# Performance work log

Measured on AMD Instinct MI355X. Metric: run time of the kernel, lower is better.

## Reference

```python
import jax, jax.numpy as jnp
import numpy as np

B, N, F_IN, E, S, L, ITERS = 1, 3072, 64, 4, 32, 3, 5  # batch, nodes, in-feats, edge types, units, layers, GGNN iters


def _gated_graph(h, edges, wz, wr, wh, uz, ur, uh, bz, br):
    # h: [B,N,S]; edges: [E,N,N] (edges[e,m,n] = edge m->n of type e); w*: [E,S,S]
    def step(h, _):
        # activation = edges.transpose(1,2) @ h  -> per-type aggregation of source-node states
        act = jnp.einsum('emn,bms->bens', edges, h)          # [B,E,N,S]
        z = jax.nn.sigmoid(jnp.einsum('bens,esk->bnk', act, wz) + h @ uz + bz)
        r = jax.nn.sigmoid(jnp.einsum('bens,esk->bnk', act, wr) + h @ ur + br)
        hh = jnp.tanh(jnp.einsum('bens,esk->bnk', act, wh) + (r * h) @ uh)
        return z * h + (1.0 - z) * hh, None
    h, _ = jax.lax.scan(step, h, None, length=ITERS)
    return h


def setup_inputs() -> dict:
    key = jax.random.key(0)
    ks = jax.random.split(key, 20)
    x_padded = jax.random.normal(ks[0], (B, N, F_IN), dtype=jnp.float32)
    x_lengths = jnp.full((B,), N, dtype=jnp.int32)
    # sparse 0/1 adjacency per edge type (graph structure), stored dense as in the original
    edges = (jax.random.uniform(ks[1], (E, N, N)) < 0.005).astype(jnp.float32)
    sd = 1.0 / np.sqrt(S)
    fc_w = jax.random.normal(ks[2], (F_IN, S), jnp.float32) / np.sqrt(F_IN)
    fc_b = jnp.zeros((S,), jnp.float32)
    wz = jax.random.normal(ks[3], (L, E, S, S), jnp.float32) * sd
    wr = jax.random.normal(ks[4], (L, E, S, S), jnp.float32) * sd
    wh = jax.random.normal(ks[5], (L, E, S, S), jnp.float32) * sd
    uz = jax.random.normal(ks[6], (L, S, S), jnp.float32) * sd
    ur = jax.random.normal(ks[7], (L, S, S), jnp.float32) * sd
    uh = jax.random.normal(ks[8], (L, S, S), jnp.float32) * sd
    bz = jnp.zeros((L, S), jnp.float32)
    br = jnp.zeros((L, S), jnp.float32)
    out_w = jax.random.normal(ks[9], (S, 5), jnp.float32) * sd
    out_b = jnp.zeros((5,), jnp.float32)
    return {"x_padded": x_padded, "x_lengths": x_lengths, "edges": edges,
            "fc_w": fc_w, "fc_b": fc_b, "wz": wz, "wr": wr, "wh": wh,
            "uz": uz, "ur": ur, "uh": uh, "bz": bz, "br": br,
            "out_w": out_w, "out_b": out_b}


def reference(x_padded, x_lengths, edges, fc_w, fc_b, wz, wr, wh, uz, ur, uh, bz, br, out_w, out_b):
    h = x_padded @ fc_w + fc_b                              # [B,N,S]
    for l in range(L):                                      # 3 stacked GatedGraph layers
        h = _gated_graph(h, edges, wz[l], wr[l], wh[l], uz[l], ur[l], uh[l], bz[l], br[l])
    y = h[:, 5] @ out_w + out_b                             # node index 5 -> [B,5]
    return jax.nn.log_softmax(y, axis=1)
```

## Files before the change

kernel.cpp:

```cpp
#include <hip/hip_runtime.h>

constexpr int N     = 3072;
constexpr int S     = 32;
constexpr int E     = 4;
constexpr int FIN   = 64;
constexpr int CAP   = 64;
constexpr int NNi   = N * N;
constexpr int DUMMY = N;
constexpr int BLK   = 256;
constexpr int TPB   = 768;
constexpr int NPB   = 12;

__device__ __forceinline__ float rl(float v, int lane) {
    return __int_as_float(__builtin_amdgcn_readlane(__float_as_int(v), lane));
}
__device__ __forceinline__ float fast_sigmoid(float x) {
    x = fminf(fmaxf(x, -30.f), 30.f);
    return 1.f / (1.f + __expf(-x));
}
__device__ __forceinline__ float fast_tanh(float x) {
    x = fminf(fmaxf(x, -15.f), 15.f);
    float e = __expf(2.f * x);
    return (e - 1.f) / (e + 1.f);
}

__device__ __forceinline__ float ld_dev(const float* p) {
    return __hip_atomic_load((float*)p, __ATOMIC_RELAXED, __HIP_MEMORY_SCOPE_AGENT);
}
__device__ __forceinline__ void st_dev(float* p, float v) {
    __hip_atomic_store(p, v, __ATOMIC_RELAXED, __HIP_MEMORY_SCOPE_AGENT);
}

__device__ __forceinline__ bool gbar(int* bar, int ph, int b) {
    __shared__ int ok;
    __syncthreads();
    if (threadIdx.x == 0) {
        int* grp  = bar + (b >> 4) * 16;
        int* root = bar + 256;
        int* go   = bar + 272;
        int old = __hip_atomic_fetch_add(grp, 1, __ATOMIC_RELAXED, __HIP_MEMORY_SCOPE_AGENT);
        if (old + 1 == ph * 16) {
            int old2 = __hip_atomic_fetch_add(root, 1, __ATOMIC_RELAXED, __HIP_MEMORY_SCOPE_AGENT);
            if (old2 + 1 == ph * 16)
                __hip_atomic_store(go, ph, __ATOMIC_RELAXED, __HIP_MEMORY_SCOPE_AGENT);
        }
        int spins = 0, okl = 1;
        while (__hip_atomic_load(go, __ATOMIC_RELAXED, __HIP_MEMORY_SCOPE_AGENT) < ph) {
            __builtin_amdgcn_s_sleep(2);
            if (++spins > 300000) { okl = 0; break; }
        }
        ok = okl;
    }
    __syncthreads();
    return ok != 0;
}

__global__ __launch_bounds__(256) void build_csr(const float* __restrict__ edges,
                                                 int* __restrict__ deg,
                                                 int* __restrict__ csr) {
    int t = blockIdx.x * 256 + threadIdx.x;
    int idx4 = t * 4;
    float4 v = *reinterpret_cast<const float4*>(edges + idx4);
    if (v.x == 0.f && v.y == 0.f && v.z == 0.f && v.w == 0.f) return;
    int e   = idx4 / NNi;
    int rem = idx4 - e * NNi;
    int m   = rem / N;
    int nb  = rem - m * N;
    float w[4] = {v.x, v.y, v.z, v.w};
    int base = e * N + nb;
    #pragma unroll
    for (int j = 0; j < 4; ++j) {
        if (w[j] != 0.f) {
            int slot = base + j;
            int pos = atomicAdd(&deg[slot], 1);
            if (pos < CAP) csr[slot * CAP + pos] = m;
        }
    }
}

struct Params {
    const float *x, *fcw, *fcb;
    const float *wz, *wr, *wh, *uz, *ur, *uh, *bz, *br;
    const float *ow, *ob;
    const int   *deg, *csr;
    int   *bar;
    float *h0, *h1, *out;
};

__global__ __launch_bounds__(TPB, 1) void fused_ggnn(Params p) {
    __shared__ __align__(16) float sW[3 * 4096];
    __shared__ __align__(16) float sU[3 * 1024];
    __shared__ float sB[64];

    const int tid  = threadIdx.x;
    const int b    = blockIdx.x;
    const int wid  = tid >> 6;
    const int lane = tid & 63;
    const int s    = lane & 31;
    const int g    = lane >> 5;
    const int n    = b * NPB + wid;

    if (tid < 32 * NPB) {
        int n0 = b * NPB + (tid >> 5);
        int s0 = tid & 31;
        float acc = p.fcb[s0];
        #pragma unroll 8
        for (int k = 0; k < FIN; ++k)
            acc = fmaf(p.x[n0 * FIN + k], p.fcw[k * S + s0], acc);
        st_dev(&p.h0[n0 * S + s0], acc);
    } else if (b == 0) {
        if (tid < 416)      st_dev(&p.h0[DUMMY * S + (tid - 384)], 0.f);
        else if (tid < 448) st_dev(&p.h1[DUMMY * S + (tid - 416)], 0.f);
    }

    const int slot1 = g * N + n;
    const int slot2 = (g + 2) * N + n;
    const int d1 = min(p.deg[slot1], CAP);
    const int d2 = min(p.deg[slot2], CAP);
    const int* __restrict__ l1 = p.csr + slot1 * CAP;
    const int* __restrict__ l2 = p.csr + slot2 * CAP;
    const int dm = max(d1, d2);

    const float* hp = p.h0;
    float*       hn = p.h1;
    float hlast = 0.f;
    int   phase = 1;

    gbar(p.bar, phase, b); phase++;

    for (int l = 0; l < 3; ++l) {
        __syncthreads();
        {
            float4* dw = (float4*)sW;
            const float4* gz = (const float4*)(p.wz + l * 4096);
            const float4* gr = (const float4*)(p.wr + l * 4096);
            const float4* gh = (const float4*)(p.wh + l * 4096);
            for (int i = tid; i < 1024; i += TPB) {
                dw[i] = gz[i]; dw[1024 + i] = gr[i]; dw[2048 + i] = gh[i];
            }
            float4* du = (float4*)sU;
            const float4* guz = (const float4*)(p.uz + l * 1024);
            const float4* gur = (const float4*)(p.ur + l * 1024);
            const float4* guh = (const float4*)(p.uh + l * 1024);
            if (tid < 256) {
                du[tid] = guz[tid]; du[256 + tid] = gur[tid]; du[512 + tid] = guh[tid];
            }
            if (tid < 64) sB[tid] = (tid < 32) ? p.bz[l * 32 + tid]
                                               : p.br[l * 32 + (tid - 32)];
        }
        __syncthreads();

        for (int it = 0; it < 5; ++it) {
            float acc0 = 0.f, acc1 = 0.f;
            for (int c = 0; c < dm; c += 4) {
                int4 ia = *reinterpret_cast<const int4*>(l1 + c);
                int4 ib = *reinterpret_cast<const int4*>(l2 + c);
                int r0 = (c + 0 < d1) ? ia.x : DUMMY;
                int r1 = (c + 1 < d1) ? ia.y : DUMMY;
                int r2 = (c + 2 < d1) ? ia.z : DUMMY;
                int r3 = (c + 3 < d1) ? ia.w : DUMMY;
                int q0 = (c + 0 < d2) ? ib.x : DUMMY;
                int q1 = (c + 1 < d2) ? ib.y : DUMMY;
                int q2 = (c + 2 < d2) ? ib.z : DUMMY;
                int q3 = (c + 3 < d2) ? ib.w : DUMMY;
                float v0 = ld_dev(hp + r0 * S + s), v1 = ld_dev(hp + r1 * S + s);
                float v2 = ld_dev(hp + r2 * S + s), v3 = ld_dev(hp + r3 * S + s);
                float u0 = ld_dev(hp + q0 * S + s), u1 = ld_dev(hp + q1 * S + s);
                float u2 = ld_dev(hp + q2 * S + s), u3 = ld_dev(hp + q3 * S + s);
                acc0 += (v0 + v1) + (v2 + v3);
                acc1 += (u0 + u1) + (u2 + u3);
            }
            const float hval = ld_dev(hp + n * S + s);

            const float* __restrict__ W1 = g ? (sW + 4096) : sW;
            const float* __restrict__ U1 = g ? (sU + 1024) : sU;
            const float* __restrict__ Wh = sW + 8192;
            float accA = sB[g * 32 + s];
            float accB = 0.f;
            float hA = 0.f, hB = 0.f;
            #pragma unroll
            for (int e = 0; e < E; ++e) {
                const float src = (e < 2) ? acc0 : acc1;
                const float* w1c = W1 + e * 1024 + s;
                const float* whc = Wh + e * 1024 + s;
                #pragma unroll
                for (int k = 0; k < 32; k += 2) {
                    float a0 = rl(src, (e & 1) * 32 + k);
                    float a1 = rl(src, (e & 1) * 32 + k + 1);
                    accA = fmaf(a0, w1c[(k)     * 32], accA);
                    accB = fmaf(a1, w1c[(k + 1) * 32], accB);
                    hA   = fmaf(a0, whc[(k)     * 32], hA);
                    hB   = fmaf(a1, whc[(k + 1) * 32], hB);
                }
            }
            #pragma unroll
            for (int k = 0; k < 32; k += 2) {
                accA = fmaf(rl(hval, k),     U1[(k)     * 32 + s], accA);
                accB = fmaf(rl(hval, k + 1), U1[(k + 1) * 32 + s], accB);
            }
            const float zr  = fast_sigmoid(accA + accB);
            const float r_s = __shfl(zr, 32 + s, 64);
            const float z_s = __shfl(zr, s, 64);
            const float rh  = r_s * hval;
            const float* __restrict__ Uh = sU + 2048;
            #pragma unroll
            for (int k = 0; k < 32; k += 2) {
                hA = fmaf(rl(rh, k),     Uh[(k)     * 32 + s], hA);
                hB = fmaf(rl(rh, k + 1), Uh[(k + 1) * 32 + s], hB);
            }
            const float hh   = fast_tanh(hA + hB);
            const float hnew = fmaf(z_s, hval - hh, hh);
            if (g == 0) st_dev(&hn[n * S + s], hnew);
            hlast = hnew;

            float* t = (float*)hp; hp = hn; hn = t;

            if (l != 2 || it != 4) {
                gbar(p.bar, phase, b); phase++;
            }
        }
    }

    if (b == 0 && wid == 5) {
        float y[5];
        #pragma unroll
        for (int j = 0; j < 5; ++j) y[j] = hlast * p.ow[s * 5 + j];
        #pragma unroll
        for (int off = 1; off < 32; off <<= 1) {
            #pragma unroll
            for (int j = 0; j < 5; ++j) y[j] += __shfl_xor(y[j], off, 64);
        }
        #pragma unroll
        for (int j = 0; j < 5; ++j) y[j] += p.ob[j];
        float m = -1e30f;
        #pragma unroll
        for (int j = 0; j < 5; ++j) m = fmaxf(m, y[j]);
        float ssum = 0.f;
        #pragma unroll
        for (int j = 0; j < 5; ++j) ssum += __expf(y[j] - m);
        float lse = m + __logf(ssum);
        #pragma unroll
        for (int j = 0; j < 5; ++j) if (lane == j) p.out[j] = y[j] - lse;
    }
}

__global__ __launch_bounds__(256) void init_h_fb(const float* __restrict__ x,
                                                 const float* __restrict__ fcw,
                                                 const float* __restrict__ fcb,
                                                 float* __restrict__ h0) {
    int t = blockIdx.x * 256 + threadIdx.x;
    int s = t & 31;
    int n = t >> 5;
    float acc = fcb[s];
    #pragma unroll 8
    for (int k = 0; k < FIN; ++k)
        acc = fmaf(x[n * FIN + k], fcw[k * S + s], acc);
    h0[n * S + s] = acc;
}

__global__ __launch_bounds__(512) void ggnn_iter_fb(
    const float* __restrict__ hprev, float* __restrict__ hnext,
    const int* __restrict__ deg, const int* __restrict__ csr,
    const float* __restrict__ wz, const float* __restrict__ wr, const float* __restrict__ wh,
    const float* __restrict__ uz, const float* __restrict__ ur, const float* __restrict__ uh,
    const float* __restrict__ bz, const float* __restrict__ br) {
    __shared__ __align__(16) float sWz[4096];
    __shared__ __align__(16) float sWr[4096];
    __shared__ __align__(16) float sWh[4096];
    __shared__ __align__(16) float sUz[1024], sUr[1024], sUh[1024];

    int tid = threadIdx.x;
    {
        float4*       dz = (float4*)sWz; const float4* gz = (const float4*)wz;
        float4*       dr = (float4*)sWr; const float4* gr = (const float4*)wr;
        float4*       dh = (float4*)sWh; const float4* gh = (const float4*)wh;
        for (int i = tid; i < 1024; i += 512) { dz[i] = gz[i]; dr[i] = gr[i]; dh[i] = gh[i]; }
        float4*       duz = (float4*)sUz; const float4* guz = (const float4*)uz;
        float4*       dur = (float4*)sUr; const float4* gur = (const float4*)ur;
        float4*       duh = (float4*)sUh; const float4* guh = (const float4*)uh;
        if (tid < 256) { duz[tid] = guz[tid]; dur[tid] = gur[tid]; duh[tid] = guh[tid]; }
    }
    __syncthreads();

    const int wid  = tid >> 6;
    const int lane = tid & 63;
    const int s    = lane & 31;
    const int g    = lane >> 5;
    const int n    = blockIdx.x * 8 + wid;

    const int d1 = min(deg[g * N + n], CAP);
    const int d2 = min(deg[(g + 2) * N + n], CAP);
    const int* __restrict__ l1 = csr + (g * N + n) * CAP;
    const int* __restrict__ l2 = csr + ((g + 2) * N + n) * CAP;
    float acc0 = 0.f, acc1 = 0.f;
    const int dmax = max(d1, d2);
    for (int i = 0; i < dmax; ++i) {
        if (i < d1) acc0 += hprev[l1[i] * S + s];
        if (i < d2) acc1 += hprev[l2[i] * S + s];
    }
    const float hval = hprev[n * S + s];

    const float* __restrict__ W1 = g ? sWr : sWz;
    const float* __restrict__ U1 = g ? sUr : sUz;
    float accA = g ? br[s] : bz[s];
    float accB = 0.f;
    float hA = 0.f, hB = 0.f;
    #pragma unroll
    for (int e = 0; e < E; ++e) {
        const float src = (e < 2) ? acc0 : acc1;
        const float* w1c = W1 + e * 1024 + s;
        const float* whc = sWh + e * 1024 + s;
        #pragma unroll
        for (int k = 0; k < 32; k += 2) {
            float a0 = rl(src, (e & 1) * 32 + k);
            float a1 = rl(src, (e & 1) * 32 + k + 1);
            accA = fmaf(a0, w1c[(k)     * 32], accA);
            accB = fmaf(a1, w1c[(k + 1) * 32], accB);
            hA   = fmaf(a0, whc[(k)     * 32], hA);
            hB   = fmaf(a1, whc[(k + 1) * 32], hB);
        }
    }
    #pragma unroll
    for (int k = 0; k < 32; k += 2) {
        accA = fmaf(rl(hval, k),     U1[(k)     * 32 + s], accA);
        accB = fmaf(rl(hval, k + 1), U1[(k + 1) * 32 + s], accB);
    }
    const float zr  = fast_sigmoid(accA + accB);
    const float r_s = __shfl(zr, 32 + s, 64);
    const float z_s = __shfl(zr, s, 64);
    const float rh  = r_s * hval;
    #pragma unroll
    for (int k = 0; k < 32; k += 2) {
        hA = fmaf(rl(rh, k),     sUh[(k)     * 32 + s], hA);
        hB = fmaf(rl(rh, k + 1), sUh[(k + 1) * 32 + s], hB);
    }
    const float hh = fast_tanh(hA + hB);
    const float hnew = fmaf(z_s, hval - hh, hh);
    if (g == 0) hnext[n * S + s] = hnew;
}

__global__ void epilogue_fb(const float* __restrict__ h,
                            const float* __restrict__ ow, const float* __restrict__ ob,
                            float* __restrict__ out) {
    int lane = threadIdx.x;
    float y = 0.f;
    if (lane < 5) {
        y = ob[lane];
        for (int k = 0; k < 32; ++k)
            y = fmaf(h[5 * S + k], ow[k * 5 + lane], y);
    }
    float m = -1e30f;
    #pragma unroll
    for (int j = 0; j < 5; ++j) m = fmaxf(m, __shfl(y, j, 64));
    float ssum = 0.f;
    #pragma unroll
    for (int j = 0; j < 5; ++j) ssum += __expf(__shfl(y, j, 64) - m);
    float lse = m + __logf(ssum);
    if (lane < 5) out[lane] = y - lse;
}

extern "C" void kernel_launch(void* const* d_in, const int* in_sizes, int n_in,
                              void* d_out, int out_size, void* d_ws, size_t ws_size,
                              hipStream_t stream) {
    const float* x     = (const float*)d_in[0];
    const float* edges = (const float*)d_in[2];
    const float* fcw   = (const float*)d_in[3];
    const float* fcb   = (const float*)d_in[4];
    const float* wz    = (const float*)d_in[5];
    const float* wr    = (const float*)d_in[6];
    const float* wh    = (const float*)d_in[7];
    const float* uz    = (const float*)d_in[8];
    const float* ur    = (const float*)d_in[9];
    const float* uh    = (const float*)d_in[10];
    const float* bz    = (const float*)d_in[11];
    const float* br    = (const float*)d_in[12];
    const float* ow    = (const float*)d_in[13];
    const float* ob    = (const float*)d_in[14];

    char* ws = (char*)d_ws;
    float* h0  = (float*)(ws);
    float* h1  = (float*)(ws + 393600);
    int*   deg = (int*)(ws + 787200);
    int*   bar = (int*)(ws + 836352);
    int*   csr = (int*)(ws + 838400);

    hipMemsetAsync(deg, 0, 49152 + 2048, stream);
    build_csr<<<36864, 256, 0, stream>>>(edges, deg, csr);

    Params p;
    p.x = x; p.fcw = fcw; p.fcb = fcb;
    p.wz = wz; p.wr = wr; p.wh = wh;
    p.uz = uz; p.ur = ur; p.uh = uh;
    p.bz = bz; p.br = br; p.ow = ow; p.ob = ob;
    p.deg = deg; p.csr = csr; p.bar = bar;
    p.h0 = h0; p.h1 = h1; p.out = (float*)d_out;

    void* args[] = { &p };
    hipError_t err = hipLaunchCooperativeKernel((const void*)fused_ggnn,
                                                dim3(BLK), dim3(TPB), args, 0, stream);
    if (err != hipSuccess) {
        init_h_fb<<<384, 256, 0, stream>>>(x, fcw, fcb, h0);
        float* ha = h0;
        float* hb = h1;
        for (int l = 0; l < 3; ++l) {
            for (int it = 0; it < 5; ++it) {
                ggnn_iter_fb<<<384, 512, 0, stream>>>(ha, hb, deg, csr,
                    wz + l * 4096, wr + l * 4096, wh + l * 4096,
                    uz + l * 1024, ur + l * 1024, uh + l * 1024,
                    bz + l * 32, br + l * 32);
                float* t = ha; ha = hb; hb = t;
            }
        }
        epilogue_fb<<<1, 64, 0, stream>>>(ha, ow, ob, (float*)d_out);
    }
}
```

Before: 464.1 us.

## Map two nodes per wave, one half-wave each, with LDS-staged GRU matvecs

Each block now runs 384 threads instead of 768. Each 64-lane wave handles two nodes, with one 32-lane half per node. That half gathers all four edge types itself and computes the z, r and candidate matvecs from activations staged in shared memory, replacing the readlane broadcasts and the cross-half shuffle. The node state stays in a register instead of being reloaded from global memory each iteration. The U matrices are now read from global memory (cache) rather than shared memory, which adds block-level syncs and more serial FMAs per thread in exchange for fewer threads and less cross-lane traffic.

```diff
diff --git a/kernel.cpp b/kernel.cpp
--- a/kernel.cpp
+++ b/kernel.cpp
@@ -8,7 +8,7 @@
 constexpr int NNi   = N * N;
 constexpr int DUMMY = N;
 constexpr int BLK   = 256;
-constexpr int TPB   = 768;
+constexpr int TPB   = 384;
 constexpr int NPB   = 12;
 
 __device__ __forceinline__ float rl(float v, int lane) {
@@ -31,8 +31,7 @@
     __hip_atomic_store(p, v, __ATOMIC_RELAXED, __HIP_MEMORY_SCOPE_AGENT);
 }
 
-__device__ __forceinline__ bool gbar(int* bar, int ph, int b) {
-    __shared__ int ok;
+__device__ __forceinline__ void gbar(int* bar, int ph, int b) {
     __syncthreads();
     if (threadIdx.x == 0) {
         int* grp  = bar + (b >> 4) * 16;
@@ -44,15 +43,13 @@
             if (old2 + 1 == ph * 16)
                 __hip_atomic_store(go, ph, __ATOMIC_RELAXED, __HIP_MEMORY_SCOPE_AGENT);
         }
-        int spins = 0, okl = 1;
+        int spins = 0;
         while (__hip_atomic_load(go, __ATOMIC_RELAXED, __HIP_MEMORY_SCOPE_AGENT) < ph) {
             __builtin_amdgcn_s_sleep(2);
-            if (++spins > 300000) { okl = 0; break; }
-        }
-        ok = okl;
+            if (++spins > 300000) break;
+        }
     }
     __syncthreads();
-    return ok != 0;
 }
 
 __global__ __launch_bounds__(256) void build_csr(const float* __restrict__ edges,
@@ -87,45 +84,77 @@
     float *h0, *h1, *out;
 };
 
+__device__ __forceinline__ float matvec(const float* __restrict__ Wg,
+                                        const float* __restrict__ Ug,
+                                        const float* __restrict__ actw,
+                                        const float* __restrict__ hw,
+                                        float bias, int s) {
+    float acc = bias, acc2 = 0.f;
+    #pragma unroll
+    for (int e = 0; e < E; ++e) {
+        const float* wc = Wg + e * 1024 + s;
+        const float* ar = actw + e * 32;
+        #pragma unroll
+        for (int k4 = 0; k4 < 8; ++k4) {
+            float4 a = *reinterpret_cast<const float4*>(ar + k4 * 4);
+            acc  = fmaf(a.x, wc[(k4 * 4 + 0) * 32], acc);
+            acc2 = fmaf(a.y, wc[(k4 * 4 + 1) * 32], acc2);
+            acc  = fmaf(a.z, wc[(k4 * 4 + 2) * 32], acc);
+            acc2 = fmaf(a.w, wc[(k4 * 4 + 3) * 32], acc2);
+        }
+    }
+    const float* uc = Ug + s;
+    #pragma unroll
+    for (int k4 = 0; k4 < 8; ++k4) {
+        float4 hv = *reinterpret_cast<const float4*>(hw + k4 * 4);
+        acc  = fmaf(hv.x, uc[(k4 * 4 + 0) * 32], acc);
+        acc2 = fmaf(hv.y, uc[(k4 * 4 + 1) * 32], acc2);
+        acc  = fmaf(hv.z, uc[(k4 * 4 + 2) * 32], acc);
+        acc2 = fmaf(hv.w, uc[(k4 * 4 + 3) * 32], acc2);
+    }
+    return acc + acc2;
+}
+
 __global__ __launch_bounds__(TPB, 1) void fused_ggnn(Params p) {
     __shared__ __align__(16) float sW[3 * 4096];
-    __shared__ __align__(16) float sU[3 * 1024];
-    __shared__ float sB[64];
+    __shared__ __align__(16) float sAct[6][2][E][32];
+    __shared__ __align__(16) float sH[6][2][32];
+    __shared__ __align__(16) float sRH[6][2][32];
 
     const int tid  = threadIdx.x;
     const int b    = blockIdx.x;
-    const int wid  = tid >> 6;
+    const int w    = tid >> 6;
     const int lane = tid & 63;
+    const int pp   = lane >> 5;
     const int s    = lane & 31;
-    const int g    = lane >> 5;
-    const int n    = b * NPB + wid;
-
-    if (tid < 32 * NPB) {
-        int n0 = b * NPB + (tid >> 5);
-        int s0 = tid & 31;
-        float acc = p.fcb[s0];
+    const int n    = b * NPB + w * 2 + pp;
+
+    float hval;
+    {
+        float acc = p.fcb[s];
         #pragma unroll 8
         for (int k = 0; k < FIN; ++k)
-            acc = fmaf(p.x[n0 * FIN + k], p.fcw[k * S + s0], acc);
-        st_dev(&p.h0[n0 * S + s0], acc);
-    } else if (b == 0) {
-        if (tid < 416)      st_dev(&p.h0[DUMMY * S + (tid - 384)], 0.f);
-        else if (tid < 448) st_dev(&p.h1[DUMMY * S + (tid - 416)], 0.f);
-    }
-
-    const int slot1 = g * N + n;
-    const int slot2 = (g + 2) * N + n;
-    const int d1 = min(p.deg[slot1], CAP);
-    const int d2 = min(p.deg[slot2], CAP);
-    const int* __restrict__ l1 = p.csr + slot1 * CAP;
-    const int* __restrict__ l2 = p.csr + slot2 * CAP;
-    const int dm = max(d1, d2);
+            acc = fmaf(p.x[n * FIN + k], p.fcw[k * S + s], acc);
+        hval = acc;
+        st_dev(&p.h0[n * S + s], acc);
+    }
+    if (b == 0) {
+        if (tid < 32)      st_dev(&p.h0[DUMMY * S + tid], 0.f);
+        else if (tid < 64) st_dev(&p.h1[DUMMY * S + (tid - 32)], 0.f);
+    }
+
+    int d[E]; const int* lst[E]; int dmx = 0;
+    #pragma unroll
+    for (int e = 0; e < E; ++e) {
+        int sl = e * N + n;
+        d[e]   = min(p.deg[sl], CAP);
+        lst[e] = p.csr + sl * CAP;
+        dmx    = max(dmx, d[e]);
+    }
 
     const float* hp = p.h0;
     float*       hn = p.h1;
-    float hlast = 0.f;
-    int   phase = 1;
-
+    int phase = 1;
     gbar(p.bar, phase, b); phase++;
 
     for (int l = 0; l < 3; ++l) {
@@ -138,93 +167,59 @@
             for (int i = tid; i < 1024; i += TPB) {
                 dw[i] = gz[i]; dw[1024 + i] = gr[i]; dw[2048 + i] = gh[i];
             }
-            float4* du = (float4*)sU;
-            const float4* guz = (const float4*)(p.uz + l * 1024);
-            const float4* gur = (const float4*)(p.ur + l * 1024);
-            const float4* guh = (const float4*)(p.uh + l * 1024);
-            if (tid < 256) {
-                du[tid] = guz[tid]; du[256 + tid] = gur[tid]; du[512 + tid] = guh[tid];
+        }
+        __syncthreads();
+
+        const float* Uz = p.uz + l * 1024;
+        const float* Ur = p.ur + l * 1024;
+        const float* Uh = p.uh + l * 1024;
+        const float  bzv = p.bz[l * 32 + s];
+        const float  brv = p.br[l * 32 + s];
+
+        for (int it = 0; it < 5; ++it) {
+            float a0 = 0.f, a1 = 0.f, a2 = 0.f, a3 = 0.f;
+            for (int c = 0; c < dmx; c += 2) {
+                int i00 = (c     < d[0]) ? lst[0][c]     : DUMMY;
+                int i01 = (c + 1 < d[0]) ? lst[0][c + 1] : DUMMY;
+                int i10 = (c     < d[1]) ? lst[1][c]     : DUMMY;
+                int i11 = (c + 1 < d[1]) ? lst[1][c + 1] : DUMMY;
+                int i20 = (c     < d[2]) ? lst[2][c]     : DUMMY;
+                int i21 = (c + 1 < d[2]) ? lst[2][c + 1] : DUMMY;
+                int i30 = (c     < d[3]) ? lst[3][c]     : DUMMY;
+                int i31 = (c + 1 < d[3]) ? lst[3][c + 1] : DUMMY;
+                float v00 = ld_dev(hp + i00 * S + s), v01 = ld_dev(hp + i01 * S + s);
+                float v10 = ld_dev(hp + i10 * S + s), v11 = ld_dev(hp + i11 * S + s);
+                float v20 = ld_dev(hp + i20 * S + s), v21 = ld_dev(hp + i21 * S + s);
+                float v30 = ld_dev(hp + i30 * S + s), v31 = ld_dev(hp + i31 * S + s);
+                a0 += v00 + v01; a1 += v10 + v11;
+                a2 += v20 + v21; a3 += v30 + v31;
             }
-            if (tid < 64) sB[tid] = (tid < 32) ? p.bz[l * 32 + tid]
-                                               : p.br[l * 32 + (tid - 32)];
-        }
-        __syncthreads();
-
-        for (int it = 0; it < 5; ++it) {
-            float acc0 = 0.f, acc1 = 0.f;
-            for (int c = 0; c < dm; c += 4) {
-                int4 ia = *reinterpret_cast<const int4*>(l1 + c);
-                int4 ib = *reinterpret_cast<const int4*>(l2 + c);
-                int r0 = (c + 0 < d1) ? ia.x : DUMMY;
-                int r1 = (c + 1 < d1) ? ia.y : DUMMY;
-                int r2 = (c + 2 < d1) ? ia.z : DUMMY;
-                int r3 = (c + 3 < d1) ? ia.w : DUMMY;
-                int q0 = (c + 0 < d2) ? ib.x : DUMMY;
-                int q1 = (c + 1 < d2) ? ib.y : DUMMY;
-                int q2 = (c + 2 < d2) ? ib.z : DUMMY;
-                int q3 = (c + 3 < d2) ? ib.w : DUMMY;
-                float v0 = ld_dev(hp + r0 * S + s), v1 = ld_dev(hp + r1 * S + s);
-                float v2 = ld_dev(hp + r2 * S + s), v3 = ld_dev(hp + r3 * S + s);
-                float u0 = ld_dev(hp + q0 * S + s), u1 = ld_dev(hp + q1 * S + s);
-                float u2 = ld_dev(hp + q2 * S + s), u3 = ld_dev(hp + q3 * S + s);
-                acc0 += (v0 + v1) + (v2 + v3);
-                acc1 += (u0 + u1) + (u2 + u3);
-            }
-            const float hval = ld_dev(hp + n * S + s);
-
-            const float* __restrict__ W1 = g ? (sW + 4096) : sW;
-            const float* __restrict__ U1 = g ? (sU + 1024) : sU;
-            const float* __restrict__ Wh = sW + 8192;
-            float accA = sB[g * 32 + s];
-            float accB = 0.f;
-            float hA = 0.f, hB = 0.f;
-            #pragma unroll
-            for (int e = 0; e < E; ++e) {
-                const float src = (e < 2) ? acc0 : acc1;
-                const float* w1c = W1 + e * 1024 + s;
-                const float* whc = Wh + e * 1024 + s;
-                #pragma unroll
-                for (int k = 0; k < 32; k += 2) {
-                    float a0 = rl(src, (e & 1) * 32 + k);
-                    float a1 = rl(src, (e & 1) * 32 + k + 1);
-                    accA = fmaf(a0, w1c[(k)     * 32], accA);
-                    accB = fmaf(a1, w1c[(k + 1) * 32], accB);
-                    hA   = fmaf(a0, whc[(k)     * 32], hA);
-                    hB   = fmaf(a1, whc[(k + 1) * 32], hB);
-                }
-            }
-            #pragma unroll
-            for (int k = 0; k < 32; k += 2) {
-                accA = fmaf(rl(hval, k),     U1[(k)     * 32 + s], accA);
-                accB = fmaf(rl(hval, k + 1), U1[(k + 1) * 32 + s], accB);
-            }
-            const float zr  = fast_sigmoid(accA + accB);
-            const float r_s = __shfl(zr, 32 + s, 64);
-            const float z_s = __shfl(zr, s, 64);
-            const float rh  = r_s * hval;
-            const float* __restrict__ Uh = sU + 2048;
-            #pragma unroll
-            for (int k = 0; k < 32; k += 2) {
-                hA = fmaf(rl(rh, k),     Uh[(k)     * 32 + s], hA);
-                hB = fmaf(rl(rh, k + 1), Uh[(k + 1) * 32 + s], hB);
-            }
-            const float hh   = fast_tanh(hA + hB);
-            const float hnew = fmaf(z_s, hval - hh, hh);
-            if (g == 0) st_dev(&hn[n * S + s], hnew);
-            hlast = hnew;
-
-            float* t = (float*)hp; hp = hn; hn = t;
-
-            if (l != 2 || it != 4) {
-                gbar(p.bar, phase, b); phase++;
-            }
-        }
-    }
-
-    if (b == 0 && wid == 5) {
+            sAct[w][pp][0][s] = a0; sAct[w][pp][1][s] = a1;
+            sAct[w][pp][2][s] = a2; sAct[w][pp][3][s] = a3;
+            sH[w][pp][s] = hval;
+            __syncthreads();
+
+            const float* actw = &sAct[w][pp][0][0];
+            const float z = fast_sigmoid(matvec(sW,        Uz, actw, &sH[w][pp][0], bzv, s));
+            const float r = fast_sigmoid(matvec(sW + 4096, Ur, actw, &sH[w][pp][0], brv, s));
+            sRH[w][pp][s] = r * hval;
+            __syncthreads();
+
+            const float hh   = fast_tanh(matvec(sW + 8192, Uh, actw, &sRH[w][pp][0], 0.f, s));
+            const float hnew = fmaf(z, hval - hh, hh);
+            st_dev(&hn[n * S + s], hnew);
+            hval = hnew;
+
+            const float* t = hp; hp = hn; hn = (float*)t;
+
+            if (l != 2 || it != 4) { gbar(p.bar, phase, b); phase++; }
+        }
+    }
+
+    if (b == 0 && w == 2 && pp == 1) {
         float y[5];
         #pragma unroll
-        for (int j = 0; j < 5; ++j) y[j] = hlast * p.ow[s * 5 + j];
+        for (int j = 0; j < 5; ++j) y[j] = hval * p.ow[s * 5 + j];
         #pragma unroll
         for (int off = 1; off < 32; off <<= 1) {
             #pragma unroll
@@ -239,8 +234,7 @@
         #pragma unroll
         for (int j = 0; j < 5; ++j) ssum += __expf(y[j] - m);
         float lse = m + __logf(ssum);
-        #pragma unroll
-        for (int j = 0; j < 5; ++j) if (lane == j) p.out[j] = y[j] - lse;
+        if (s < 5) p.out[s] = y[s] - lse;
     }
 }
 
```

After: 573.4 us. 23.5% more time.
